# Performance work log

Measured on AMD Instinct MI355X. Metric: run time of the kernel, lower is better.

Reference implementation:

```python
import jax, jax.numpy as jnp
import numpy as np

SIZE = 1024
LATENT_DIM = 256
BETA_C = 0.25
LEGACY = True


def setup_inputs() -> dict:
    key = jax.random.key(0)
    k1, k2 = jax.random.split(key)
    z = jax.random.normal(k1, (8, LATENT_DIM, 16, 16, 16), dtype=jnp.float32)
    # nn.Embedding weight initialized uniform(-1/size, 1/size)
    embedding = jax.random.uniform(
        k2, (SIZE, LATENT_DIM), minval=-1.0 / SIZE, maxval=1.0 / SIZE, dtype=jnp.float32
    )
    return {"z": z, "embedding": embedding}


def reference(z, embedding):
    sg = jax.lax.stop_gradient
    B, C, D, H, W = z.shape
    # [B, D, H, W, C]
    zp = jnp.transpose(z, (0, 2, 3, 4, 1))
    zf = zp.reshape(-1, C)  # [N, C]
    # pairwise squared distances [N, K]
    d = (
        jnp.sum(zf * zf, axis=1, keepdims=True)
        + jnp.sum(embedding * embedding, axis=1)
        - 2.0 * (zf @ embedding.T)
    )
    idx = jnp.argmin(d, axis=1)  # [N]
    # direct gather == one-hot @ embedding
    z_q = embedding[idx].reshape(zp.shape)
    if LEGACY:
        loss = jnp.mean((sg(z_q) - zp) ** 2) + BETA_C * jnp.mean((z_q - sg(zp)) ** 2)
    else:
        loss = BETA_C * jnp.mean((sg(z_q) - zp) ** 2) + jnp.mean((z_q - sg(zp)) ** 2)
    # perplexity: e_mean = mean of one-hot encodings == normalized counts
    counts = jnp.zeros((SIZE,), dtype=z.dtype).at[idx].add(1.0)
    e_mean = counts / zf.shape[0]
    perplexity = jnp.exp(-jnp.sum(e_mean * jnp.log(e_mean + 1e-10)))
    # straight-through estimator
    z_q = zp + sg(z_q - zp)
    z_q = jnp.transpose(z_q, (0, 4, 1, 2, 3))  # back to [B, C, D, H, W]
    return z_q, loss, perplexity, idx
```

## Files before the change

### kernel.cpp

```cpp
#include <hip/hip_runtime.h>
#include <cstddef>
#include <cstdint>

#define CDIM 256
#define SPAT 4096
#define KCODE 1024

#define LOSS_OFF 8388608
#define PERP_OFF 8388609
#define IDX_OFF  8388610

typedef __bf16 bf16x8 __attribute__((ext_vector_type(8)));
typedef float floatx16 __attribute__((ext_vector_type(16)));
typedef unsigned short ushort8 __attribute__((ext_vector_type(8)));

__device__ __forceinline__ unsigned short f2bf_rne(float f) {
    union { float f; uint32_t u; } c; c.f = f;
    uint32_t u = c.u;
    return (unsigned short)((u + 0x7fffu + ((u >> 16) & 1u)) >> 16);
}
__device__ __forceinline__ float bf2f(unsigned short h) {
    union { float f; uint32_t u; } c; c.u = ((uint32_t)h) << 16;
    return c.f;
}

__device__ __forceinline__ void dma16(const void* g, void* l) {
    __builtin_amdgcn_global_load_lds(
        (const __attribute__((address_space(1))) void*)g,
        (__attribute__((address_space(3))) void*)l, 16, 0, 0);
}

__global__ __launch_bounds__(256) void vq_prep(const float* __restrict__ emb,
                                               unsigned short* __restrict__ ehsw,
                                               unsigned short* __restrict__ elsw,
                                               float* __restrict__ enorm,
                                               float* __restrict__ counts,
                                               float* __restrict__ losssum) {
    int tid = threadIdx.x;
    if (blockIdx.x == 0) {
        for (int i = tid; i < KCODE; i += 256) counts[i] = 0.0f;
        if (tid == 0) losssum[0] = 0.0f;
    }
    int w = tid >> 6, lane = tid & 63;
    int k = blockIdx.x * 4 + w;
    const float* row = emb + (size_t)k * CDIM;
    float s = 0.0f;
#pragma unroll
    for (int i = 0; i < 4; ++i) {
        float v = row[lane + 64 * i];
        s = fmaf(v, v, s);
    }
#pragma unroll
    for (int m = 32; m > 0; m >>= 1) s += __shfl_xor(s, m, 64);
    if (lane == 0) enorm[k] = s;

    float4 v4 = *(const float4*)(row + lane * 4);
    unsigned short h0 = f2bf_rne(v4.x), h1 = f2bf_rne(v4.y),
                   h2 = f2bf_rne(v4.z), h3 = f2bf_rne(v4.w);
    ushort4 hv = make_ushort4(h0, h1, h2, h3);
    ushort4 lv = make_ushort4(f2bf_rne(v4.x - bf2f(h0)), f2bf_rne(v4.y - bf2f(h1)),
                              f2bf_rne(v4.z - bf2f(h2)), f2bf_rne(v4.w - bf2f(h3)));
    int kb = lane >> 1, cj = (lane & 1) * 4;
    int st = k >> 5, ks = k & 31;
    int phys = kb ^ (ks & 7);
    size_t dst = (size_t)st * 8192 + ks * 256 + phys * 8 + cj;
    *(ushort4*)(ehsw + dst) = hv;
    *(ushort4*)(elsw + dst) = lv;
}

__global__ __launch_bounds__(256, 1) void vq_main(const float* __restrict__ z,
                                                  const float* __restrict__ emb,
                                                  const unsigned short* __restrict__ ehsw,
                                                  const unsigned short* __restrict__ elsw,
                                                  const float* __restrict__ enorm,
                                                  float* __restrict__ counts,
                                                  float* __restrict__ losssum,
                                                  float* __restrict__ out) {
    __shared__ __align__(16) unsigned char lds[131072 + 4096 + 512 + 1024 + 1024 + 512];
    float* zhalf = (float*)lds;
    float* ens_s = (float*)(lds + 131072);
    float* zzs   = (float*)(lds + 135168);
    float* pb_s  = (float*)(lds + 135680);
    int*   pb_i  = (int*)(lds + 136704);
    int*   bidxs = (int*)(lds + 137728);

    const int tid = threadIdx.x;
    const int w = tid >> 6;
    const int lane = tid & 63;
    const int m_ = lane & 31;
    const int g = lane >> 5;
    const int kh = w >> 1;
    const int cw = w & 1;
    const int n0 = blockIdx.x * 128;
    const int b = n0 >> 12;
    const int sp0 = n0 & 4095;
    const float* zb = z + (size_t)b * CDIM * SPAT + sp0;

    ushort8 zh0[16], zl0[16], zh1[16], zl1[16];

    for (int h = 0; h < 2; ++h) {
        for (int i = tid; i < CDIM * 16; i += 256) {
            int c = i >> 4, seg = i & 15;
            *(float4*)&zhalf[c * 64 + seg * 4] =
                *(const float4*)(zb + (size_t)c * SPAT + h * 64 + seg * 4);
        }
        __syncthreads();
        if (cw == h) {
#pragma unroll
            for (int t = 0; t < 2; ++t) {
#pragma unroll
                for (int kc = 0; kc < 16; ++kc) {
#pragma unroll
                    for (int j = 0; j < 8; ++j) {
                        float v = zhalf[(kc * 16 + g * 8 + j) * 64 + t * 32 + m_];
                        unsigned short hb = f2bf_rne(v);
                        unsigned short lb = f2bf_rne(v - bf2f(hb));
                        if (t == 0) { zh0[kc][j] = hb; zl0[kc][j] = lb; }
                        else        { zh1[kc][j] = hb; zl1[kc][j] = lb; }
                    }
                }
            }
        } else if (kh == 0) {
            float s = 0.0f;
            for (int c = 0; c < CDIM; ++c) {
                float v = zhalf[c * 64 + lane];
                s = fmaf(v, v, s);
            }
            zzs[h * 64 + lane] = s;
        } else if (h == 0) {
            for (int i = lane; i < KCODE; i += 64) ens_s[i] = enorm[i];
        }
        __syncthreads();
    }

    const float zzv0 = zzs[cw * 64 + m_];
    const float zzv1 = zzs[cw * 64 + 32 + m_];

    float bs0 = 3.4e38f, bs1 = 3.4e38f;
    int bi0 = 0, bi1 = 0;

    const char* gsrc = (const char*)((w & 1) ? elsw : ehsw);

    {
        const char* gp = gsrc + ((size_t)(kh * 16) << 14) + (lane << 4);
        char* lp = (char*)lds + ((size_t)w << 14);
#pragma unroll
        for (int j = 0; j < 16; ++j) dma16(gp + j * 1024, lp + j * 1024);
    }

    for (int s = 0; s < 16; ++s) {
        __syncthreads();
        if (s < 15) {
            const char* gp = gsrc + ((size_t)(kh * 16 + s + 1) << 14) + (lane << 4);
            char* lp = (char*)lds + (((size_t)(s + 1) & 1) << 16) + ((size_t)w << 14);
#pragma unroll
            for (int j = 0; j < 16; ++j) dma16(gp + j * 1024, lp + j * 1024);
            __builtin_amdgcn_sched_barrier(0);
        }
        const char* EHb = (const char*)lds + (((size_t)s & 1) << 16) + ((size_t)kh << 15);
        const char* ELb = EHb + 16384;

        floatx16 a0 = {0.0f, 0.0f, 0.0f, 0.0f, 0.0f, 0.0f, 0.0f, 0.0f,
                       0.0f, 0.0f, 0.0f, 0.0f, 0.0f, 0.0f, 0.0f, 0.0f};
        floatx16 a1 = a0;
#pragma unroll
        for (int kc = 0; kc < 16; ++kc) {
            int kb0 = kc * 2 + g;
            int off = m_ * 512 + ((kb0 ^ (m_ & 7)) << 4);
            bf16x8 aeh = *(const bf16x8*)(EHb + off);
            bf16x8 ael = *(const bf16x8*)(ELb + off);
            bf16x8 bh0 = __builtin_bit_cast(bf16x8, zh0[kc]);
            bf16x8 bl0 = __builtin_bit_cast(bf16x8, zl0[kc]);
            bf16x8 bh1 = __builtin_bit_cast(bf16x8, zh1[kc]);
            bf16x8 bl1 = __builtin_bit_cast(bf16x8, zl1[kc]);
            a0 = __builtin_amdgcn_mfma_f32_32x32x16_bf16(aeh, bh0, a0, 0, 0, 0);
            a1 = __builtin_amdgcn_mfma_f32_32x32x16_bf16(aeh, bh1, a1, 0, 0, 0);
            a0 = __builtin_amdgcn_mfma_f32_32x32x16_bf16(ael, bh0, a0, 0, 0, 0);
            a1 = __builtin_amdgcn_mfma_f32_32x32x16_bf16(ael, bh1, a1, 0, 0, 0);
            a0 = __builtin_amdgcn_mfma_f32_32x32x16_bf16(aeh, bl0, a0, 0, 0, 0);
            a1 = __builtin_amdgcn_mfma_f32_32x32x16_bf16(aeh, bl1, a1, 0, 0, 0);
        }

#pragma unroll
        for (int reg = 0; reg < 16; ++reg) {
            int mm = (reg & 3) + 8 * (reg >> 2) + 4 * g;
            int code = kh * 512 + s * 32 + mm;
            float en = ens_s[code];
            float d0 = (zzv0 + en) - 2.0f * a0[reg];
            float d1 = (zzv1 + en) - 2.0f * a1[reg];
            if (d0 < bs0) { bs0 = d0; bi0 = code; }
            if (d1 < bs1) { bs1 = d1; bi1 = code; }
        }
    }

    {
        float s2 = __shfl_xor(bs0, 32, 64);
        int i2 = __shfl_xor(bi0, 32, 64);
        if (s2 < bs0 || (s2 == bs0 && i2 < bi0)) { bs0 = s2; bi0 = i2; }
        float s3 = __shfl_xor(bs1, 32, 64);
        int i3 = __shfl_xor(bi1, 32, 64);
        if (s3 < bs1 || (s3 == bs1 && i3 < bi1)) { bs1 = s3; bi1 = i3; }
    }
    __syncthreads();
    if (lane < 32) {
        pb_s[kh * 128 + cw * 64 + m_] = bs0;
        pb_s[kh * 128 + cw * 64 + 32 + m_] = bs1;
        pb_i[kh * 128 + cw * 64 + m_] = bi0;
        pb_i[kh * 128 + cw * 64 + 32 + m_] = bi1;
    }
    __syncthreads();
    if (tid < 128) {
        float s0 = pb_s[tid], s1 = pb_s[128 + tid];
        int i0 = pb_i[tid], i1 = pb_i[128 + tid];
        int ki = (s1 < s0) ? i1 : i0;
        bidxs[tid] = ki;
        out[IDX_OFF + n0 + tid] = (float)ki;
        atomicAdd(&counts[ki], 1.0f);
    }
    __syncthreads();

    float ls = 0.0f;
    float* outz = out + (size_t)b * CDIM * SPAT + sp0;
    const int col4 = tid & 31;
    const int c_0 = tid >> 5;
    int k0 = bidxs[col4 * 4 + 0];
    int k1 = bidxs[col4 * 4 + 1];
    int k2 = bidxs[col4 * 4 + 2];
    int k3 = bidxs[col4 * 4 + 3];
    const float* e0 = emb + (size_t)k0 * CDIM;
    const float* e1 = emb + (size_t)k1 * CDIM;
    const float* e2 = emb + (size_t)k2 * CDIM;
    const float* e3 = emb + (size_t)k3 * CDIM;
    for (int c = c_0; c < CDIM; c += 8) {
        float4 zp = *(const float4*)(zb + (size_t)c * SPAT + col4 * 4);
        float d0 = e0[c] - zp.x, d1 = e1[c] - zp.y,
              d2 = e2[c] - zp.z, d3 = e3[c] - zp.w;
        float4 o;
        o.x = zp.x + d0; o.y = zp.y + d1; o.z = zp.z + d2; o.w = zp.w + d3;
        ls = fmaf(d0, d0, ls); ls = fmaf(d1, d1, ls);
        ls = fmaf(d2, d2, ls); ls = fmaf(d3, d3, ls);
        *(float4*)(outz + (size_t)c * SPAT + col4 * 4) = o;
    }
#pragma unroll
    for (int m = 32; m > 0; m >>= 1) ls += __shfl_xor(ls, m, 64);
    if (lane == 0) atomicAdd(losssum, ls);
}

__global__ __launch_bounds__(256) void vq_finalize(const float* __restrict__ counts,
                                                   const float* __restrict__ losssum,
                                                   float* __restrict__ out) {
    __shared__ float red[256];
    int tid = threadIdx.x;
    float s = 0.0f;
    for (int k = tid; k < KCODE; k += 256) {
        float em = counts[k] * (1.0f / 32768.0f);
        s += em * logf(em + 1e-10f);
    }
    red[tid] = s;
    __syncthreads();
    for (int off = 128; off > 0; off >>= 1) {
        if (tid < off) red[tid] += red[tid + off];
        __syncthreads();
    }
    if (tid == 0) {
        float m = losssum[0] * (1.0f / 8388608.0f);
        out[LOSS_OFF] = m + 0.25f * m;
        out[PERP_OFF] = expf(-red[0]);
    }
}

extern "C" void kernel_launch(void* const* d_in, const int* in_sizes, int n_in,
                              void* d_out, int out_size, void* d_ws, size_t ws_size,
                              hipStream_t stream) {
    const float* z = (const float*)d_in[0];
    const float* emb = (const float*)d_in[1];
    float* out = (float*)d_out;
    unsigned short* ehsw = (unsigned short*)d_ws;
    unsigned short* elsw = ehsw + (size_t)KCODE * CDIM;
    float* enorm = (float*)(elsw + (size_t)KCODE * CDIM);
    float* counts = enorm + KCODE;
    float* losssum = counts + KCODE;

    vq_prep<<<256, 256, 0, stream>>>(emb, ehsw, elsw, enorm, counts, losssum);
    vq_main<<<256, 256, 0, stream>>>(z, emb, ehsw, elsw, enorm, counts, losssum, out);
    vq_finalize<<<1, 256, 0, stream>>>(counts, losssum, out);
}
```

Baseline: 172.3 us.

## Split main kernel into ping-pong wave groups alternating MFMA compute and DMA

Doubles the block to 512 threads and splits the waves into two parity groups. On each codebook stage one group runs the MFMA distance tile and argmin while the other issues the global-to-LDS DMA for the next stage, which is meant to overlap loading with compute inside the CU. The prep kernel now writes a transposed codebook layout with no XOR swizzle, so each lane reads consecutive 16-byte chunks without bank conflicts. The final argmin now merges four partial results per column. Launch bounds of (512,2) cap registers per thread while each thread still holds large register arrays of split z fragments, so heavy spilling is a real risk.

```diff
diff --git a/kernel.cpp b/kernel.cpp
--- a/kernel.cpp
+++ b/kernel.cpp
@@ -12,7 +12,7 @@
 
 typedef __bf16 bf16x8 __attribute__((ext_vector_type(8)));
 typedef float floatx16 __attribute__((ext_vector_type(16)));
-typedef unsigned short ushort8 __attribute__((ext_vector_type(8)));
+typedef unsigned short us8 __attribute__((ext_vector_type(8)));
 
 __device__ __forceinline__ unsigned short f2bf_rne(float f) {
     union { float f; uint32_t u; } c; c.f = f;
@@ -61,14 +61,13 @@
     ushort4 lv = make_ushort4(f2bf_rne(v4.x - bf2f(h0)), f2bf_rne(v4.y - bf2f(h1)),
                               f2bf_rne(v4.z - bf2f(h2)), f2bf_rne(v4.w - bf2f(h3)));
     int kb = lane >> 1, cj = (lane & 1) * 4;
-    int st = k >> 5, ks = k & 31;
-    int phys = kb ^ (ks & 7);
-    size_t dst = (size_t)st * 8192 + ks * 256 + phys * 8 + cj;
+    int kh = k >> 9, st = (k >> 5) & 15, ks = k & 31;
+    size_t dst = (size_t)(st * 2 + kh) * 8192 + kb * 256 + ks * 8 + cj;
     *(ushort4*)(ehsw + dst) = hv;
     *(ushort4*)(elsw + dst) = lv;
 }
 
-__global__ __launch_bounds__(256, 1) void vq_main(const float* __restrict__ z,
+__global__ __launch_bounds__(512, 2) void vq_main(const float* __restrict__ z,
                                                   const float* __restrict__ emb,
                                                   const unsigned short* __restrict__ ehsw,
                                                   const unsigned short* __restrict__ elsw,
@@ -76,30 +75,31 @@
                                                   float* __restrict__ counts,
                                                   float* __restrict__ losssum,
                                                   float* __restrict__ out) {
-    __shared__ __align__(16) unsigned char lds[131072 + 4096 + 512 + 1024 + 1024 + 512];
+    __shared__ __align__(16) unsigned char lds[131072 + 4096 + 512 + 2048 + 2048 + 512];
     float* zhalf = (float*)lds;
     float* ens_s = (float*)(lds + 131072);
     float* zzs   = (float*)(lds + 135168);
     float* pb_s  = (float*)(lds + 135680);
-    int*   pb_i  = (int*)(lds + 136704);
-    int*   bidxs = (int*)(lds + 137728);
+    int*   pb_i  = (int*)(lds + 137728);
+    int*   bidxs = (int*)(lds + 139776);
 
     const int tid = threadIdx.x;
     const int w = tid >> 6;
     const int lane = tid & 63;
     const int m_ = lane & 31;
     const int g = lane >> 5;
-    const int kh = w >> 1;
+    const int par = w >> 2;
+    const int kh = (w >> 1) & 1;
     const int cw = w & 1;
     const int n0 = blockIdx.x * 128;
     const int b = n0 >> 12;
     const int sp0 = n0 & 4095;
     const float* zb = z + (size_t)b * CDIM * SPAT + sp0;
 
-    ushort8 zh0[16], zl0[16], zh1[16], zl1[16];
+    us8 zh0[16], zl0[16], zh1[16], zl1[16];
 
     for (int h = 0; h < 2; ++h) {
-        for (int i = tid; i < CDIM * 16; i += 256) {
+        for (int i = tid; i < CDIM * 16; i += 512) {
             int c = i >> 4, seg = i & 15;
             *(float4*)&zhalf[c * 64 + seg * 4] =
                 *(const float4*)(zb + (size_t)c * SPAT + h * 64 + seg * 4);
@@ -120,14 +120,14 @@
                     }
                 }
             }
-        } else if (kh == 0) {
+        } else if (kh == 0 && par == 0) {
             float s = 0.0f;
             for (int c = 0; c < CDIM; ++c) {
                 float v = zhalf[c * 64 + lane];
                 s = fmaf(v, v, s);
             }
             zzs[h * 64 + lane] = s;
-        } else if (h == 0) {
+        } else if (kh == 1 && par == 0 && h == 0) {
             for (int i = lane; i < KCODE; i += 64) ens_s[i] = enorm[i];
         }
         __syncthreads();
@@ -139,57 +139,57 @@
     float bs0 = 3.4e38f, bs1 = 3.4e38f;
     int bi0 = 0, bi1 = 0;
 
-    const char* gsrc = (const char*)((w & 1) ? elsw : ehsw);
-
-    {
-        const char* gp = gsrc + ((size_t)(kh * 16) << 14) + (lane << 4);
-        char* lp = (char*)lds + ((size_t)w << 14);
+    const char* gsrc = (const char*)(cw ? elsw : ehsw);
+
+    if (par == 0) {
+        const char* gp = gsrc + ((size_t)kh << 14) + (lane << 4);
+        char* lp = (char*)lds + ((size_t)kh << 15) + ((size_t)cw << 14);
 #pragma unroll
         for (int j = 0; j < 16; ++j) dma16(gp + j * 1024, lp + j * 1024);
     }
 
     for (int s = 0; s < 16; ++s) {
         __syncthreads();
-        if (s < 15) {
-            const char* gp = gsrc + ((size_t)(kh * 16 + s + 1) << 14) + (lane << 4);
-            char* lp = (char*)lds + (((size_t)(s + 1) & 1) << 16) + ((size_t)w << 14);
+        if ((s & 1) == par) {
+            const char* EHb = (const char*)lds + (((size_t)s & 1) << 16) + ((size_t)kh << 15);
+            const char* ELb = EHb + 16384;
+
+            floatx16 a0 = {0.0f, 0.0f, 0.0f, 0.0f, 0.0f, 0.0f, 0.0f, 0.0f,
+                           0.0f, 0.0f, 0.0f, 0.0f, 0.0f, 0.0f, 0.0f, 0.0f};
+            floatx16 a1 = a0;
+#pragma unroll
+            for (int kc = 0; kc < 16; ++kc) {
+                int kb0 = kc * 2 + g;
+                int off = kb0 * 512 + m_ * 16;
+                bf16x8 aeh = *(const bf16x8*)(EHb + off);
+                bf16x8 ael = *(const bf16x8*)(ELb + off);
+                bf16x8 bh0 = __builtin_bit_cast(bf16x8, zh0[kc]);
+                bf16x8 bl0 = __builtin_bit_cast(bf16x8, zl0[kc]);
+                bf16x8 bh1 = __builtin_bit_cast(bf16x8, zh1[kc]);
+                bf16x8 bl1 = __builtin_bit_cast(bf16x8, zl1[kc]);
+                a0 = __builtin_amdgcn_mfma_f32_32x32x16_bf16(aeh, bh0, a0, 0, 0, 0);
+                a1 = __builtin_amdgcn_mfma_f32_32x32x16_bf16(aeh, bh1, a1, 0, 0, 0);
+                a0 = __builtin_amdgcn_mfma_f32_32x32x16_bf16(ael, bh0, a0, 0, 0, 0);
+                a1 = __builtin_amdgcn_mfma_f32_32x32x16_bf16(ael, bh1, a1, 0, 0, 0);
+                a0 = __builtin_amdgcn_mfma_f32_32x32x16_bf16(aeh, bl0, a0, 0, 0, 0);
+                a1 = __builtin_amdgcn_mfma_f32_32x32x16_bf16(aeh, bl1, a1, 0, 0, 0);
+            }
+#pragma unroll
+            for (int reg = 0; reg < 16; ++reg) {
+                int mm = (reg & 3) + 8 * (reg >> 2) + 4 * g;
+                int code = kh * 512 + s * 32 + mm;
+                float en = ens_s[code];
+                float d0 = (zzv0 + en) - 2.0f * a0[reg];
+                float d1 = (zzv1 + en) - 2.0f * a1[reg];
+                if (d0 < bs0) { bs0 = d0; bi0 = code; }
+                if (d1 < bs1) { bs1 = d1; bi1 = code; }
+            }
+        } else if (s < 15) {
+            const char* gp = gsrc + ((size_t)((s + 1) * 2 + kh) << 14) + (lane << 4);
+            char* lp = (char*)lds + (((size_t)(s + 1) & 1) << 16)
+                       + ((size_t)kh << 15) + ((size_t)cw << 14);
 #pragma unroll
             for (int j = 0; j < 16; ++j) dma16(gp + j * 1024, lp + j * 1024);
-            __builtin_amdgcn_sched_barrier(0);
-        }
-        const char* EHb = (const char*)lds + (((size_t)s & 1) << 16) + ((size_t)kh << 15);
-        const char* ELb = EHb + 16384;
-
-        floatx16 a0 = {0.0f, 0.0f, 0.0f, 0.0f, 0.0f, 0.0f, 0.0f, 0.0f,
-                       0.0f, 0.0f, 0.0f, 0.0f, 0.0f, 0.0f, 0.0f, 0.0f};
-        floatx16 a1 = a0;
-#pragma unroll
-        for (int kc = 0; kc < 16; ++kc) {
-            int kb0 = kc * 2 + g;
-            int off = m_ * 512 + ((kb0 ^ (m_ & 7)) << 4);
-            bf16x8 aeh = *(const bf16x8*)(EHb + off);
-            bf16x8 ael = *(const bf16x8*)(ELb + off);
-            bf16x8 bh0 = __builtin_bit_cast(bf16x8, zh0[kc]);
-            bf16x8 bl0 = __builtin_bit_cast(bf16x8, zl0[kc]);
-            bf16x8 bh1 = __builtin_bit_cast(bf16x8, zh1[kc]);
-            bf16x8 bl1 = __builtin_bit_cast(bf16x8, zl1[kc]);
-            a0 = __builtin_amdgcn_mfma_f32_32x32x16_bf16(aeh, bh0, a0, 0, 0, 0);
-            a1 = __builtin_amdgcn_mfma_f32_32x32x16_bf16(aeh, bh1, a1, 0, 0, 0);
-            a0 = __builtin_amdgcn_mfma_f32_32x32x16_bf16(ael, bh0, a0, 0, 0, 0);
-            a1 = __builtin_amdgcn_mfma_f32_32x32x16_bf16(ael, bh1, a1, 0, 0, 0);
-            a0 = __builtin_amdgcn_mfma_f32_32x32x16_bf16(aeh, bl0, a0, 0, 0, 0);
-            a1 = __builtin_amdgcn_mfma_f32_32x32x16_bf16(aeh, bl1, a1, 0, 0, 0);
-        }
-
-#pragma unroll
-        for (int reg = 0; reg < 16; ++reg) {
-            int mm = (reg & 3) + 8 * (reg >> 2) + 4 * g;
-            int code = kh * 512 + s * 32 + mm;
-            float en = ens_s[code];
-            float d0 = (zzv0 + en) - 2.0f * a0[reg];
-            float d1 = (zzv1 + en) - 2.0f * a1[reg];
-            if (d0 < bs0) { bs0 = d0; bi0 = code; }
-            if (d1 < bs1) { bs1 = d1; bi1 = code; }
         }
     }
 
@@ -203,16 +203,22 @@
     }
     __syncthreads();
     if (lane < 32) {
-        pb_s[kh * 128 + cw * 64 + m_] = bs0;
-        pb_s[kh * 128 + cw * 64 + 32 + m_] = bs1;
-        pb_i[kh * 128 + cw * 64 + m_] = bi0;
-        pb_i[kh * 128 + cw * 64 + 32 + m_] = bi1;
+        int r = par * 2 + kh;
+        pb_s[r * 128 + cw * 64 + m_] = bs0;
+        pb_s[r * 128 + cw * 64 + 32 + m_] = bs1;
+        pb_i[r * 128 + cw * 64 + m_] = bi0;
+        pb_i[r * 128 + cw * 64 + 32 + m_] = bi1;
     }
     __syncthreads();
     if (tid < 128) {
-        float s0 = pb_s[tid], s1 = pb_s[128 + tid];
-        int i0 = pb_i[tid], i1 = pb_i[128 + tid];
-        int ki = (s1 < s0) ? i1 : i0;
+        float s = pb_s[tid];
+        int ki = pb_i[tid];
+#pragma unroll
+        for (int r = 1; r < 4; ++r) {
+            float s2 = pb_s[r * 128 + tid];
+            int k2 = pb_i[r * 128 + tid];
+            if (s2 < s || (s2 == s && k2 < ki)) { s = s2; ki = k2; }
+        }
         bidxs[tid] = ki;
         out[IDX_OFF + n0 + tid] = (float)ki;
         atomicAdd(&counts[ki], 1.0f);
@@ -231,7 +237,7 @@
     const float* e1 = emb + (size_t)k1 * CDIM;
     const float* e2 = emb + (size_t)k2 * CDIM;
     const float* e3 = emb + (size_t)k3 * CDIM;
-    for (int c = c_0; c < CDIM; c += 8) {
+    for (int c = c_0; c < CDIM; c += 16) {
         float4 zp = *(const float4*)(zb + (size_t)c * SPAT + col4 * 4);
         float d0 = e0[c] - zp.x, d1 = e1[c] - zp.y,
               d2 = e2[c] - zp.z, d3 = e3[c] - zp.w;
@@ -282,6 +288,6 @@
     float* losssum = counts + KCODE;
 
     vq_prep<<<256, 256, 0, stream>>>(emb, ehsw, elsw, enorm, counts, losssum);
-    vq_main<<<256, 256, 0, stream>>>(z, emb, ehsw, elsw, enorm, counts, losssum, out);
+    vq_main<<<256, 512, 0, stream>>>(z, emb, ehsw, elsw, enorm, counts, losssum, out);
     vq_finalize<<<1, 256, 0, stream>>>(counts, losssum, out);
 }
```

Measured after the change: 284.1 us. +64.9%, slower.

## Read codebook MFMA fragments directly from global memory and keep z tile in LDS

Applied to the files above, without the earlier changes.

Prep now stores the bf16 hi/lo codebook in a fragment-major layout, so each lane loads its MFMA A-operand with a single coalesced 16-byte global load. This replaces the double-buffered global-to-LDS DMA pipeline and its per-stage barriers. Both z halves stay resident in LDS, so the epilogue reads z from LDS instead of re-reading global memory. The argmin merge across the two halves also gains lowest-index tie-breaking. The cost is that codebook loads now go through L2/L1 with no explicit prefetch overlap, which may expose latency in the MFMA loop.

```diff
diff --git a/kernel.cpp b/kernel.cpp
--- a/kernel.cpp
+++ b/kernel.cpp
@@ -12,7 +12,7 @@
 
 typedef __bf16 bf16x8 __attribute__((ext_vector_type(8)));
 typedef float floatx16 __attribute__((ext_vector_type(16)));
-typedef unsigned short ushort8 __attribute__((ext_vector_type(8)));
+typedef unsigned short us8 __attribute__((ext_vector_type(8)));
 
 __device__ __forceinline__ unsigned short f2bf_rne(float f) {
     union { float f; uint32_t u; } c; c.f = f;
@@ -24,15 +24,9 @@
     return c.f;
 }
 
-__device__ __forceinline__ void dma16(const void* g, void* l) {
-    __builtin_amdgcn_global_load_lds(
-        (const __attribute__((address_space(1))) void*)g,
-        (__attribute__((address_space(3))) void*)l, 16, 0, 0);
-}
-
 __global__ __launch_bounds__(256) void vq_prep(const float* __restrict__ emb,
-                                               unsigned short* __restrict__ ehsw,
-                                               unsigned short* __restrict__ elsw,
+                                               unsigned short* __restrict__ eht,
+                                               unsigned short* __restrict__ elt,
                                                float* __restrict__ enorm,
                                                float* __restrict__ counts,
                                                float* __restrict__ losssum) {
@@ -60,24 +54,25 @@
     ushort4 hv = make_ushort4(h0, h1, h2, h3);
     ushort4 lv = make_ushort4(f2bf_rne(v4.x - bf2f(h0)), f2bf_rne(v4.y - bf2f(h1)),
                               f2bf_rne(v4.z - bf2f(h2)), f2bf_rne(v4.w - bf2f(h3)));
-    int kb = lane >> 1, cj = (lane & 1) * 4;
-    int st = k >> 5, ks = k & 31;
-    int phys = kb ^ (ks & 7);
-    size_t dst = (size_t)st * 8192 + ks * 256 + phys * 8 + cj;
-    *(ushort4*)(ehsw + dst) = hv;
-    *(ushort4*)(elsw + dst) = lv;
+    int kc = lane >> 2;
+    int g = (lane >> 1) & 1;
+    int cj = (lane & 1) * 4;
+    int m_ = k & 31, cb = (k >> 5) & 15, kh = k >> 9;
+    size_t dst = (size_t)(((kh * 16 + cb) * 16 + kc)) * 512 + (g * 32 + m_) * 8 + cj;
+    *(ushort4*)(eht + dst) = hv;
+    *(ushort4*)(elt + dst) = lv;
 }
 
 __global__ __launch_bounds__(256, 1) void vq_main(const float* __restrict__ z,
                                                   const float* __restrict__ emb,
-                                                  const unsigned short* __restrict__ ehsw,
-                                                  const unsigned short* __restrict__ elsw,
+                                                  const unsigned short* __restrict__ eht,
+                                                  const unsigned short* __restrict__ elt,
                                                   const float* __restrict__ enorm,
                                                   float* __restrict__ counts,
                                                   float* __restrict__ losssum,
                                                   float* __restrict__ out) {
     __shared__ __align__(16) unsigned char lds[131072 + 4096 + 512 + 1024 + 1024 + 512];
-    float* zhalf = (float*)lds;
+    float* zt    = (float*)lds;
     float* ens_s = (float*)(lds + 131072);
     float* zzs   = (float*)(lds + 135168);
     float* pb_s  = (float*)(lds + 135680);
@@ -96,9 +91,10 @@
     const int sp0 = n0 & 4095;
     const float* zb = z + (size_t)b * CDIM * SPAT + sp0;
 
-    ushort8 zh0[16], zl0[16], zh1[16], zl1[16];
+    us8 zh0[16], zl0[16], zh1[16], zl1[16];
 
     for (int h = 0; h < 2; ++h) {
+        float* zhalf = zt + h * 16384;
         for (int i = tid; i < CDIM * 16; i += 256) {
             int c = i >> 4, seg = i & 15;
             *(float4*)&zhalf[c * 64 + seg * 4] =
@@ -139,36 +135,19 @@
     float bs0 = 3.4e38f, bs1 = 3.4e38f;
     int bi0 = 0, bi1 = 0;
 
-    const char* gsrc = (const char*)((w & 1) ? elsw : ehsw);
-
-    {
-        const char* gp = gsrc + ((size_t)(kh * 16) << 14) + (lane << 4);
-        char* lp = (char*)lds + ((size_t)w << 14);
-#pragma unroll
-        for (int j = 0; j < 16; ++j) dma16(gp + j * 1024, lp + j * 1024);
-    }
-
-    for (int s = 0; s < 16; ++s) {
-        __syncthreads();
-        if (s < 15) {
-            const char* gp = gsrc + ((size_t)(kh * 16 + s + 1) << 14) + (lane << 4);
-            char* lp = (char*)lds + (((size_t)(s + 1) & 1) << 16) + ((size_t)w << 14);
-#pragma unroll
-            for (int j = 0; j < 16; ++j) dma16(gp + j * 1024, lp + j * 1024);
-            __builtin_amdgcn_sched_barrier(0);
-        }
-        const char* EHb = (const char*)lds + (((size_t)s & 1) << 16) + ((size_t)kh << 15);
-        const char* ELb = EHb + 16384;
-
+    const us8* Ah = (const us8*)eht + ((size_t)kh << 14) + lane;
+    const us8* Al = (const us8*)elt + ((size_t)kh << 14) + lane;
+
+    for (int cb = 0; cb < 16; ++cb) {
         floatx16 a0 = {0.0f, 0.0f, 0.0f, 0.0f, 0.0f, 0.0f, 0.0f, 0.0f,
                        0.0f, 0.0f, 0.0f, 0.0f, 0.0f, 0.0f, 0.0f, 0.0f};
         floatx16 a1 = a0;
 #pragma unroll
         for (int kc = 0; kc < 16; ++kc) {
-            int kb0 = kc * 2 + g;
-            int off = m_ * 512 + ((kb0 ^ (m_ & 7)) << 4);
-            bf16x8 aeh = *(const bf16x8*)(EHb + off);
-            bf16x8 ael = *(const bf16x8*)(ELb + off);
+            us8 ehu = Ah[(cb * 16 + kc) * 64];
+            us8 elu = Al[(cb * 16 + kc) * 64];
+            bf16x8 aeh = __builtin_bit_cast(bf16x8, ehu);
+            bf16x8 ael = __builtin_bit_cast(bf16x8, elu);
             bf16x8 bh0 = __builtin_bit_cast(bf16x8, zh0[kc]);
             bf16x8 bl0 = __builtin_bit_cast(bf16x8, zl0[kc]);
             bf16x8 bh1 = __builtin_bit_cast(bf16x8, zh1[kc]);
@@ -180,11 +159,10 @@
             a0 = __builtin_amdgcn_mfma_f32_32x32x16_bf16(aeh, bl0, a0, 0, 0, 0);
             a1 = __builtin_amdgcn_mfma_f32_32x32x16_bf16(aeh, bl1, a1, 0, 0, 0);
         }
-
 #pragma unroll
         for (int reg = 0; reg < 16; ++reg) {
             int mm = (reg & 3) + 8 * (reg >> 2) + 4 * g;
-            int code = kh * 512 + s * 32 + mm;
+            int code = kh * 512 + cb * 32 + mm;
             float en = ens_s[code];
             float d0 = (zzv0 + en) - 2.0f * a0[reg];
             float d1 = (zzv1 + en) - 2.0f * a1[reg];
@@ -210,9 +188,11 @@
     }
     __syncthreads();
     if (tid < 128) {
-        float s0 = pb_s[tid], s1 = pb_s[128 + tid];
-        int i0 = pb_i[tid], i1 = pb_i[128 + tid];
-        int ki = (s1 < s0) ? i1 : i0;
+        float s = pb_s[tid];
+        int ki = pb_i[tid];
+        float s2 = pb_s[128 + tid];
+        int k2 = pb_i[128 + tid];
+        if (s2 < s || (s2 == s && k2 < ki)) { s = s2; ki = k2; }
         bidxs[tid] = ki;
         out[IDX_OFF + n0 + tid] = (float)ki;
         atomicAdd(&counts[ki], 1.0f);
@@ -223,6 +203,8 @@
     float* outz = out + (size_t)b * CDIM * SPAT + sp0;
     const int col4 = tid & 31;
     const int c_0 = tid >> 5;
+    const int hh = col4 >> 4;
+    const int lc = (col4 & 15) * 4;
     int k0 = bidxs[col4 * 4 + 0];
     int k1 = bidxs[col4 * 4 + 1];
     int k2 = bidxs[col4 * 4 + 2];
@@ -232,7 +214,7 @@
     const float* e2 = emb + (size_t)k2 * CDIM;
     const float* e3 = emb + (size_t)k3 * CDIM;
     for (int c = c_0; c < CDIM; c += 8) {
-        float4 zp = *(const float4*)(zb + (size_t)c * SPAT + col4 * 4);
+        float4 zp = *(const float4*)&zt[hh * 16384 + c * 64 + lc];
         float d0 = e0[c] - zp.x, d1 = e1[c] - zp.y,
               d2 = e2[c] - zp.z, d3 = e3[c] - zp.w;
         float4 o;
@@ -275,13 +257,13 @@
     const float* z = (const float*)d_in[0];
     const float* emb = (const float*)d_in[1];
     float* out = (float*)d_out;
-    unsigned short* ehsw = (unsigned short*)d_ws;
-    unsigned short* elsw = ehsw + (size_t)KCODE * CDIM;
-    float* enorm = (float*)(elsw + (size_t)KCODE * CDIM);
+    unsigned short* eht = (unsigned short*)d_ws;
+    unsigned short* elt = eht + (size_t)KCODE * CDIM;
+    float* enorm = (float*)(elt + (size_t)KCODE * CDIM);
     float* counts = enorm + KCODE;
     float* losssum = counts + KCODE;
 
-    vq_prep<<<256, 256, 0, stream>>>(emb, ehsw, elsw, enorm, counts, losssum);
-    vq_main<<<256, 256, 0, stream>>>(z, emb, ehsw, elsw, enorm, counts, losssum, out);
+    vq_prep<<<256, 256, 0, stream>>>(emb, eht, elt, enorm, counts, losssum);
+    vq_main<<<256, 256, 0, stream>>>(z, emb, eht, elt, enorm, counts, losssum, out);
     vq_finalize<<<1, 256, 0, stream>>>(counts, losssum, out);
 }
```

Result: slower. 216.8 us (+25.8%).
